# Optimization experiments

Hardware: AMD Instinct MI355X
Metric: run time of the kernel (lower is better)

The kernel has to match this reference:

```python
import jax, jax.numpy as jnp
import numpy as np

C_IN, C_OUT, K = 64, 64, 3
KK = K * K


def _conv3x3(x, w, b):
    # x: [B, Cin, H, W], w: [Cout, Cin, 3, 3], b: [Cout] or None. stride 1, pad 1.
    y = jax.lax.conv_general_dilated(
        x, w, window_strides=(1, 1), padding=((1, 1), (1, 1)),
        dimension_numbers=("NCHW", "OIHW", "NCHW"))
    if b is not None:
        y = y + b[None, :, None, None]
    return y


def _deform_conv2d(x, offset, mask, weight):
    # torchvision.ops.deform_conv2d with stride=1, pad=1, dilation=1, 1 offset group.
    # x: [B,C,H,W]; offset: [B,2*KK,H,W] (per-tap (dy,dx)); mask: [B,KK,H,W];
    # weight: [O,C,K,K]
    B, C, H, W = x.shape
    O = weight.shape[0]
    ky, kx = jnp.meshgrid(jnp.arange(K), jnp.arange(K), indexing="ij")
    hs = jnp.arange(H)
    ws = jnp.arange(W)
    # base sample positions per tap k=(ky*K+kx): [KK,H,W]
    base_y = (hs[:, None] - 1)[None] + ky.reshape(KK, 1, 1)
    base_x = (ws[None, :] - 1)[None] + kx.reshape(KK, 1, 1)
    off = offset.reshape(B, KK, 2, H, W)
    py = base_y[None].astype(x.dtype) + off[:, :, 0]  # [B,KK,H,W]
    px = base_x[None].astype(x.dtype) + off[:, :, 1]

    y0 = jnp.floor(py)
    x0 = jnp.floor(px)
    wy = py - y0  # bilinear fractional weights
    wx = px - x0
    y0i = y0.astype(jnp.int32)
    x0i = x0.astype(jnp.int32)

    imflat = x.reshape(B, C, H * W)

    def gather_b(im, idx):  # im: [C,HW], idx: [KK,H,W] -> [C,KK,H,W]
        return im[:, idx]

    val = jnp.zeros((B, C, KK, H, W), x.dtype)
    for dy, dx in ((0, 0), (0, 1), (1, 0), (1, 1)):
        yc = y0i + dy
        xc = x0i + dx
        valid = ((yc >= 0) & (yc < H) & (xc >= 0) & (xc < W)).astype(x.dtype)
        cw = (wy if dy else (1.0 - wy)) * (wx if dx else (1.0 - wx)) * valid
        idx = jnp.clip(yc, 0, H - 1) * W + jnp.clip(xc, 0, W - 1)
        g = jax.vmap(gather_b)(imflat, idx)  # [B,C,KK,H,W]
        val = val + cw[:, None] * g
    val = val * mask[:, None]  # modulation
    # contract 9-tap patches with conv weight
    return jnp.einsum("bckhw,ock->bohw", val, weight.reshape(O, C, KK))


def setup_inputs() -> dict:
    key = jax.random.key(0)
    ks = jax.random.split(key, 8)
    B, H, W = 4, 96, 96
    cin2 = 2 * C_IN + 2
    frame_i = jax.random.normal(ks[0], (B, C_IN, H, W), jnp.float32)
    frame_j = jax.random.normal(ks[1], (B, C_IN, H, W), jnp.float32)
    flow_ij = jax.random.normal(ks[2], (B, 2, H, W), jnp.float32)
    # small random weights so offsets are nonzero (zero-init would degenerate)
    w_off = jax.random.normal(ks[3], (2 * KK, cin2, K, K), jnp.float32) * 0.01
    b_off = jax.random.normal(ks[4], (2 * KK,), jnp.float32) * 0.1
    w_mod = jax.random.normal(ks[5], (KK, cin2, K, K), jnp.float32) * 0.01
    b_mod = jax.random.normal(ks[6], (KK,), jnp.float32) * 0.1
    w_reg = jax.random.normal(ks[7], (C_OUT, C_IN, K, K), jnp.float32) * (1.0 / np.sqrt(C_IN * KK))
    return {"frame_i": frame_i, "frame_j": frame_j, "flow_ij": flow_ij,
            "w_off": w_off, "b_off": b_off, "w_mod": w_mod, "b_mod": b_mod,
            "w_reg": w_reg}


def reference(frame_i, frame_j, flow_ij, w_off, b_off, w_mod, b_mod, w_reg):
    offset_input = jnp.concatenate([frame_i, frame_j, flow_ij], axis=1)
    offset = _conv3x3(offset_input, w_off, b_off)            # [B,2*KK,H,W]
    modulator = 2.0 * jax.nn.sigmoid(_conv3x3(offset_input, w_mod, b_mod))  # [B,KK,H,W]
    return _deform_conv2d(frame_j, offset, modulator, w_reg)
```

## Files before the change

kernel.cpp:

```cpp
#include <hip/hip_runtime.h>
#include <math.h>

#define BB   4
#define HH   96
#define WW   96
#define HW   (HH * WW)
#define CIN  64
#define COUT 64
#define C2B  192
#define NROW (BB * HW)
#define ZROW NROW
#define NSTRIP (NROW / 16)
#define BPX3 (NSTRIP / 8)
#define NA   (9 * 5 * 2 * 512)
#define NW   (9 * 2 * 4 * 512)
#define PXB2 (NROW / 32)
#define PWBLK 324
#define TSX  35
#define PR   55

typedef short v8s __attribute__((ext_vector_type(8)));
typedef float v4f __attribute__((ext_vector_type(4)));

__device__ __forceinline__ unsigned short f2bf(float f) {
    unsigned u = __float_as_uint(f);
    return (unsigned short)((u + 0x7FFFu + ((u >> 16) & 1u)) >> 16);
}
__device__ __forceinline__ unsigned pack2(float a, float b) {
    return (unsigned)f2bf(a) | ((unsigned)f2bf(b) << 16);
}
__device__ __forceinline__ unsigned bil2(unsigned a, unsigned b, unsigned c,
                                         unsigned d, float w00, float w01,
                                         float w10, float w11) {
    float lo = w00 * __uint_as_float(a << 16) + w01 * __uint_as_float(b << 16)
             + w10 * __uint_as_float(c << 16) + w11 * __uint_as_float(d << 16);
    float hi = w00 * __uint_as_float(a & 0xffff0000u)
             + w01 * __uint_as_float(b & 0xffff0000u)
             + w10 * __uint_as_float(c & 0xffff0000u)
             + w11 * __uint_as_float(d & 0xffff0000u);
    return pack2(lo, hi);
}

__global__ __launch_bounds__(256) void prep_kernel(
    const float* __restrict__ fi, const float* __restrict__ fj,
    const float* __restrict__ fl, const float* __restrict__ w_off,
    const float* __restrict__ w_mod, const float* __restrict__ w_reg,
    unsigned short* __restrict__ xt, unsigned short* __restrict__ wa2f,
    unsigned short* __restrict__ wb2f, uint4* __restrict__ vt)
{
    int blk = blockIdx.x;
    if (blk < PXB2) {
        __shared__ __align__(16) unsigned tile[64 * TSX];
        int tid = threadIdx.x;
        int p = tid & 63, cg = tid >> 6;
        int u = blk >> 1, half = blk & 1;
        int r0 = u * 64;
        int b = r0 / HW;
        int hwb = r0 - b * HW;
        int hw = hwb + p;
        uint4* dst = (uint4*)(xt + (size_t)r0 * C2B);
        if (half == 0) {
            const float* pi = fi + (size_t)b * CIN * HW + hw;
#pragma unroll
            for (int d = 0; d < 8; ++d) {
                int c = cg * 16 + 2 * d;
                tile[p * TSX + cg * 8 + d] =
                    pack2(pi[(size_t)c * HW], pi[(size_t)(c + 1) * HW]);
            }
            __syncthreads();
#pragma unroll
            for (int i = 0; i < 2; ++i) {
                int gq = i * 256 + tid;
                int rl = gq >> 3, c4 = gq & 7;
                const unsigned* s = &tile[rl * TSX + c4 * 4];
                uint4 v = {s[0], s[1], s[2], s[3]};
                dst[rl * 24 + c4] = v;
            }
        } else {
            const float* pj = fj + (size_t)b * CIN * HW + hw;
#pragma unroll
            for (int d = 0; d < 8; ++d) {
                int c = cg * 16 + 2 * d;
                tile[p * TSX + cg * 8 + d] =
                    pack2(pj[(size_t)c * HW], pj[(size_t)(c + 1) * HW]);
            }
            if (cg == 0) {
                const float* pf = fl + (size_t)b * 2 * HW + hw;
                tile[p * TSX + 32] = pack2(pf[0], pf[HW]);
            }
            __syncthreads();
#pragma unroll
            for (int i = 0; i < 4; ++i) {
                int gq = i * 256 + tid;
                int rl = gq >> 4, c4 = gq & 15;
                uint4 v = {0u, 0u, 0u, 0u};
                if (c4 < 8) {
                    const unsigned* s = &tile[rl * TSX + c4 * 4];
                    v.x = s[0]; v.y = s[1]; v.z = s[2]; v.w = s[3];
                } else if (c4 == 8) {
                    v.x = tile[rl * TSX + 32];
                }
                int pc4 = (c4 < 8) ? ((c4 & 3) * 2 + (c4 >> 2)) : c4;
                dst[rl * 24 + 8 + pc4] = v;
            }
#pragma unroll
            for (int i = 0; i < 2; ++i) {
                int it = i * 256 + tid;
                int pl = it >> 6, rl = it & 63;
                int o  = (pl >> 1) + (pl & 1) * 4;
                const unsigned* s = &tile[rl * TSX + o * 4];
                uint4 v = {s[0], s[1], s[2], s[3]};
                vt[((size_t)(b * 8 + pl)) * HW + hwb + rl] = v;
            }
        }
    } else if (blk < PXB2 + PWBLK) {
        int e = (blk - PXB2) * 256 + threadIdx.x;
        if (e < NA) {
            int t  = e / 5120;
            int r1 = e - t * 5120;
            int ks = r1 >> 10;
            int r2 = r1 & 1023;
            int nt = r2 >> 9;
            int l9 = r2 & 511;
            int l  = l9 >> 3, ee = l9 & 7;
            int m  = l & 15, g = l >> 4;
            int oc = nt * 16 + m;
            int ch = ks * 32 + g * 8 + ee;
            float v = 0.0f;
            if (oc < 27 && ch < 130) {
                if (oc < 18) v = w_off[((size_t)oc * 130 + ch) * 9 + t];
                else         v = w_mod[((size_t)(oc - 18) * 130 + ch) * 9 + t];
            }
            wa2f[e] = f2bf(v);
        } else {
            int e2 = e - NA;
            if (e2 < NW) {
                int k  = e2 >> 12;
                int r1 = e2 & 4095;
                int ks = r1 >> 11;
                int r2 = r1 & 2047;
                int nt = r2 >> 9;
                int l9 = r2 & 511;
                int l  = l9 >> 3, ee = l9 & 7;
                int m  = l & 15, g = l >> 4;
                int o  = nt * 16 + m;
                int c  = ks * 32 + g * 8 + ee;
                wb2f[e2] = f2bf(w_reg[((size_t)o * 64 + c) * 9 + k]);
            }
        }
    } else {
        if (threadIdx.x < 24) {
            uint4 z = {0u, 0u, 0u, 0u};
            ((uint4*)(xt + (size_t)ZROW * C2B))[threadIdx.x] = z;
        }
    }
}

__global__ __launch_bounds__(512, 4) void fused_kernel(
    const unsigned short* __restrict__ xt,
    const unsigned short* __restrict__ wa2f,
    const unsigned short* __restrict__ wb2f,
    const uint4* __restrict__ vt,
    const float* __restrict__ b_off, const float* __restrict__ b_mod,
    float* __restrict__ out)
{
    __shared__ __align__(16) unsigned char pool[32768];
    __shared__ __align__(16) float red1[8][8][64];
    __shared__ float lraw[16 * 28];

    uint4* patch4 = (uint4*)pool;
    float* red2   = (float*)pool;

    int l = threadIdx.x & 63;
    int wid = __builtin_amdgcn_readfirstlane(threadIdx.x >> 6);
    int m = l & 15, g = l >> 4;
    int strip = (blockIdx.x & 7) * BPX3 + (blockIdx.x >> 3);
    int b = strip / (HW / 16);
    int hw0 = (strip - b * (HW / 16)) * 16;
    int hw = hw0 + m;
    int x = hw % WW, y = hw / WW;
    int y0b = hw0 / WW, x0b = hw0 - y0b * WW;

#pragma unroll
    for (int i = 0; i < 3; ++i) {
        int item = i * 512 + threadIdx.x;
        if (item < 1080) {
            int run = item / 360;
            int rem = item - run * 360;
            int r18 = rem / 20;
            int c8  = rem - r18 * 20;
            int yy = y0b + run - 1;
            int xx = x0b - 1 + r18;
            bool ok = ((unsigned)yy < HH) && ((unsigned)xx < WW);
            uint4 v = {0u, 0u, 0u, 0u};
            if (ok)
                v = ((const uint4*)(xt + (size_t)(b * HW + yy * WW + xx) * C2B))[c8];
            patch4[c8 * PR + run * 18 + r18] = v;
        }
    }
    __syncthreads();

    v4f acc0 = {0.f, 0.f, 0.f, 0.f};
    v4f acc1 = {0.f, 0.f, 0.f, 0.f};
    {
        int nu = (wid < 5) ? 6 : 5;
#pragma unroll
        for (int i = 0; i < 6; ++i) {
            if (i < nu) {
                int u = wid + 8 * i;
                int t = u / 5, ks = u - 5 * t;
                int r = (t / 3) * 18 + (t % 3) + m;
                int c8 = (ks == 0) ? g : (ks == 1) ? 4 + g
                       : (ks == 2) ? 8 + 2 * g : (ks == 3) ? 9 + 2 * g
                       : 16 + g;
                v8s a = *(const v8s*)&patch4[c8 * PR + r];
                const unsigned short* wp =
                    wa2f + ((size_t)(u * 2)) * 512 + l * 8;
                v8s b0 = *(const v8s*)(wp);
                v8s b1 = *(const v8s*)(wp + 512);
                acc0 = __builtin_amdgcn_mfma_f32_16x16x32_bf16(a, b0, acc0, 0, 0, 0);
                acc1 = __builtin_amdgcn_mfma_f32_16x16x32_bf16(a, b1, acc1, 0, 0, 0);
            }
        }
    }

    {
#pragma unroll
        for (int j = 0; j < 4; ++j) red1[wid][j][l] = acc0[j];
#pragma unroll
        for (int j = 0; j < 4; ++j) red1[wid][4 + j][l] = acc1[j];
    }
    __syncthreads();

    {
        int j = wid;
        float v = 0.f;
#pragma unroll
        for (int sw = 0; sw < 8; ++sw) v += red1[sw][j][l];
        int r = j & 3;
        int oc = (j < 4) ? m : 16 + m;
        int pos = g * 4 + r;
        if (oc < 18) {
            lraw[pos * 28 + oc] = v + b_off[oc];
        } else if (oc < 27) {
            lraw[pos * 28 + oc] =
                2.0f / (1.0f + __expf(-(v + b_mod[oc - 18])));
        }
    }
    __syncthreads();

    v4f acc[4];
#pragma unroll
    for (int nt = 0; nt < 4; ++nt) acc[nt] = (v4f){0.f, 0.f, 0.f, 0.f};

    const uint4* p0 = vt + ((size_t)(b * 8 + 2 * g + 0)) * HW;
    const uint4* p1 = vt + ((size_t)(b * 8 + 2 * g + 1)) * HW;

    auto do_tap = [&](int k) {
        int ky = k / 3, kx = k - 3 * ky;
        float dy = lraw[m * 28 + 2 * k];
        float dx = lraw[m * 28 + 2 * k + 1];
        float mm = lraw[m * 28 + 18 + k];

        float py = (float)(y - 1 + ky) + dy;
        float px = (float)(x - 1 + kx) + dx;
        float fy = floorf(py), fx = floorf(px);
        int   y0 = (int)fy,    x0 = (int)fx;
        float wy = py - fy,    wx = px - fx;
        int   y1 = y0 + 1,     x1 = x0 + 1;

        bool y0v = (y0 >= 0) && (y0 < HH);
        bool y1v = (y1 >= 0) && (y1 < HH);
        bool x0v = (x0 >= 0) && (x0 < WW);
        bool x1v = (x1 >= 0) && (x1 < WW);

        float w00 = (1.f - wy) * (1.f - wx) * ((y0v && x0v) ? mm : 0.f);
        float w01 = (1.f - wy) * wx         * ((y0v && x1v) ? mm : 0.f);
        float w10 = wy * (1.f - wx)         * ((y1v && x0v) ? mm : 0.f);
        float w11 = wy * wx                 * ((y1v && x1v) ? mm : 0.f);

        int y0c = min(max(y0, 0), HH - 1), y1c = min(max(y1, 0), HH - 1);
        int x0c = min(max(x0, 0), WW - 1), x1c = min(max(x1, 0), WW - 1);
        int i00 = y0c * WW + x0c, i01 = y0c * WW + x1c;
        int i10 = y1c * WW + x0c, i11 = y1c * WW + x1c;

        uint4 a00 = p0[i00];
        uint4 a01 = p0[i01];
        uint4 a10 = p0[i10];
        uint4 a11 = p0[i11];
        uint4 c00 = p1[i00];
        uint4 c01 = p1[i01];
        uint4 c10 = p1[i10];
        uint4 c11 = p1[i11];

        uint4 ov0, ov1;
        ov0.x = bil2(a00.x, a01.x, a10.x, a11.x, w00, w01, w10, w11);
        ov0.y = bil2(a00.y, a01.y, a10.y, a11.y, w00, w01, w10, w11);
        ov0.z = bil2(a00.z, a01.z, a10.z, a11.z, w00, w01, w10, w11);
        ov0.w = bil2(a00.w, a01.w, a10.w, a11.w, w00, w01, w10, w11);
        ov1.x = bil2(c00.x, c01.x, c10.x, c11.x, w00, w01, w10, w11);
        ov1.y = bil2(c00.y, c01.y, c10.y, c11.y, w00, w01, w10, w11);
        ov1.z = bil2(c00.z, c01.z, c10.z, c11.z, w00, w01, w10, w11);
        ov1.w = bil2(c00.w, c01.w, c10.w, c11.w, w00, w01, w10, w11);
        v8s af0 = __builtin_bit_cast(v8s, ov0);
        v8s af1 = __builtin_bit_cast(v8s, ov1);

#pragma unroll
        for (int nt = 0; nt < 4; ++nt) {
            const unsigned short* wp0 =
                wb2f + ((size_t)((k * 2 + 0) * 4 + nt)) * 512 + l * 8;
            const unsigned short* wp1 =
                wb2f + ((size_t)((k * 2 + 1) * 4 + nt)) * 512 + l * 8;
            v8s bb0 = *(const v8s*)wp0;
            v8s bb1 = *(const v8s*)wp1;
            acc[nt] = __builtin_amdgcn_mfma_f32_16x16x32_bf16(af0, bb0, acc[nt], 0, 0, 0);
            acc[nt] = __builtin_amdgcn_mfma_f32_16x16x32_bf16(af1, bb1, acc[nt], 0, 0, 0);
        }
    };

    do_tap(wid);
    if (wid == 7) do_tap(8);

    {
#pragma unroll
        for (int nt = 0; nt < 4; ++nt)
#pragma unroll
            for (int r = 0; r < 4; ++r)
                red2[((size_t)wid * 16 + nt * 4 + r) * 64 + l] = acc[nt][r];
    }
    __syncthreads();
    {
        int nt = wid >> 1, r0 = (wid & 1) * 2;
        float v0 = 0.f, v1 = 0.f;
#pragma unroll
        for (int sw = 0; sw < 8; ++sw) {
            v0 += red2[((size_t)sw * 16 + nt * 4 + r0) * 64 + l];
            v1 += red2[((size_t)sw * 16 + nt * 4 + r0 + 1) * 64 + l];
        }
        float* op = out + ((size_t)(b * COUT + nt * 16 + m)) * HW
                  + hw0 + g * 4 + r0;
        float2 s2 = {v0, v1};
        *(float2*)op = s2;
    }
}

extern "C" void kernel_launch(void* const* d_in, const int* in_sizes, int n_in,
                              void* d_out, int out_size, void* d_ws, size_t ws_size,
                              hipStream_t stream)
{
    const float* frame_i = (const float*)d_in[0];
    const float* frame_j = (const float*)d_in[1];
    const float* flow_ij = (const float*)d_in[2];
    const float* w_off   = (const float*)d_in[3];
    const float* b_off   = (const float*)d_in[4];
    const float* w_mod   = (const float*)d_in[5];
    const float* b_mod   = (const float*)d_in[6];
    const float* w_reg   = (const float*)d_in[7];
    float* out = (float*)d_out;

    unsigned short* xt   = (unsigned short*)d_ws;
    unsigned short* wa2f = xt + (size_t)(NROW + 1) * C2B;
    unsigned short* wb2f = wa2f + NA;
    uint4* vt            = (uint4*)(wb2f + NW);

    prep_kernel<<<PXB2 + PWBLK + 1, 256, 0, stream>>>(
        frame_i, frame_j, flow_ij, w_off, w_mod, w_reg, xt, wa2f, wb2f, vt);

    fused_kernel<<<NSTRIP, 512, 0, stream>>>(
        xt, wa2f, wb2f, vt, b_off, b_mod, out);
}
```

Before: 115.5 us.

## Shrink shared pool, split tap 8 across two waves, two-stage reduction

```diff
diff --git a/kernel.cpp b/kernel.cpp
--- a/kernel.cpp
+++ b/kernel.cpp
@@ -156,7 +156,7 @@
     }
 }
 
-__global__ __launch_bounds__(512, 4) void fused_kernel(
+__global__ __launch_bounds__(512, 8) void fused_kernel(
     const unsigned short* __restrict__ xt,
     const unsigned short* __restrict__ wa2f,
     const unsigned short* __restrict__ wb2f,
@@ -164,7 +164,7 @@
     const float* __restrict__ b_off, const float* __restrict__ b_mod,
     float* __restrict__ out)
 {
-    __shared__ __align__(16) unsigned char pool[32768];
+    __shared__ __align__(16) unsigned char pool[17600];
     __shared__ __align__(16) float red1[8][8][64];
     __shared__ float lraw[16 * 28];
 
@@ -253,9 +253,6 @@
 #pragma unroll
     for (int nt = 0; nt < 4; ++nt) acc[nt] = (v4f){0.f, 0.f, 0.f, 0.f};
 
-    const uint4* p0 = vt + ((size_t)(b * 8 + 2 * g + 0)) * HW;
-    const uint4* p1 = vt + ((size_t)(b * 8 + 2 * g + 1)) * HW;
-
     auto do_tap = [&](int k) {
         int ky = k / 3, kx = k - 3 * ky;
         float dy = lraw[m * 28 + 2 * k];
@@ -283,6 +280,9 @@
         int x0c = min(max(x0, 0), WW - 1), x1c = min(max(x1, 0), WW - 1);
         int i00 = y0c * WW + x0c, i01 = y0c * WW + x1c;
         int i10 = y1c * WW + x0c, i11 = y1c * WW + x1c;
+
+        const uint4* p0 = vt + ((size_t)(b * 8 + 2 * g + 0)) * HW;
+        const uint4* p1 = vt + ((size_t)(b * 8 + 2 * g + 1)) * HW;
 
         uint4 a00 = p0[i00];
         uint4 a01 = p0[i01];
@@ -318,24 +318,87 @@
         }
     };
 
+    auto do_half = [&](int k, int ks) {
+        int ky = k / 3, kx = k - 3 * ky;
+        float dy = lraw[m * 28 + 2 * k];
+        float dx = lraw[m * 28 + 2 * k + 1];
+        float mm = lraw[m * 28 + 18 + k];
+
+        float py = (float)(y - 1 + ky) + dy;
+        float px = (float)(x - 1 + kx) + dx;
+        float fy = floorf(py), fx = floorf(px);
+        int   y0 = (int)fy,    x0 = (int)fx;
+        float wy = py - fy,    wx = px - fx;
+        int   y1 = y0 + 1,     x1 = x0 + 1;
+
+        bool y0v = (y0 >= 0) && (y0 < HH);
+        bool y1v = (y1 >= 0) && (y1 < HH);
+        bool x0v = (x0 >= 0) && (x0 < WW);
+        bool x1v = (x1 >= 0) && (x1 < WW);
+
+        float w00 = (1.f - wy) * (1.f - wx) * ((y0v && x0v) ? mm : 0.f);
+        float w01 = (1.f - wy) * wx         * ((y0v && x1v) ? mm : 0.f);
+        float w10 = wy * (1.f - wx)         * ((y1v && x0v) ? mm : 0.f);
+        float w11 = wy * wx                 * ((y1v && x1v) ? mm : 0.f);
+
+        int y0c = min(max(y0, 0), HH - 1), y1c = min(max(y1, 0), HH - 1);
+        int x0c = min(max(x0, 0), WW - 1), x1c = min(max(x1, 0), WW - 1);
+        int i00 = y0c * WW + x0c, i01 = y0c * WW + x1c;
+        int i10 = y1c * WW + x0c, i11 = y1c * WW + x1c;
+
+        const uint4* pk = vt + ((size_t)(b * 8 + 2 * g + ks)) * HW;
+        uint4 a00 = pk[i00];
+        uint4 a01 = pk[i01];
+        uint4 a10 = pk[i10];
+        uint4 a11 = pk[i11];
+
+        uint4 ov;
+        ov.x = bil2(a00.x, a01.x, a10.x, a11.x, w00, w01, w10, w11);
+        ov.y = bil2(a00.y, a01.y, a10.y, a11.y, w00, w01, w10, w11);
+        ov.z = bil2(a00.z, a01.z, a10.z, a11.z, w00, w01, w10, w11);
+        ov.w = bil2(a00.w, a01.w, a10.w, a11.w, w00, w01, w10, w11);
+        v8s af = __builtin_bit_cast(v8s, ov);
+
+#pragma unroll
+        for (int nt = 0; nt < 4; ++nt) {
+            const unsigned short* wp =
+                wb2f + ((size_t)((k * 2 + ks) * 4 + nt)) * 512 + l * 8;
+            v8s bb = *(const v8s*)wp;
+            acc[nt] = __builtin_amdgcn_mfma_f32_16x16x32_bf16(af, bb, acc[nt], 0, 0, 0);
+        }
+    };
+
     do_tap(wid);
-    if (wid == 7) do_tap(8);
-
-    {
+    if (wid == 6) do_half(8, 0);
+    if (wid == 7) do_half(8, 1);
+
+    if (wid >= 4) {
+        float* rb = red2 + ((size_t)(wid - 4) * 16) * 64;
 #pragma unroll
         for (int nt = 0; nt < 4; ++nt)
 #pragma unroll
             for (int r = 0; r < 4; ++r)
-                red2[((size_t)wid * 16 + nt * 4 + r) * 64 + l] = acc[nt][r];
+                rb[(nt * 4 + r) * 64 + l] = acc[nt][r];
+    }
+    __syncthreads();
+    if (wid < 4) {
+        float* rb = red2 + ((size_t)wid * 16) * 64;
+#pragma unroll
+        for (int nt = 0; nt < 4; ++nt)
+#pragma unroll
+            for (int r = 0; r < 4; ++r) {
+                float t = rb[(nt * 4 + r) * 64 + l] + acc[nt][r];
+                rb[(nt * 4 + r) * 64 + l] = t;
+            }
     }
     __syncthreads();
     {
         int nt = wid >> 1, r0 = (wid & 1) * 2;
         float v0 = 0.f, v1 = 0.f;
 #pragma unroll
-        for (int sw = 0; sw < 8; ++sw) {
-            v0 += red2[((size_t)sw * 16 + nt * 4 + r0) * 64 + l];
-            v1 += red2[((size_t)sw * 16 + nt * 4 + r0 + 1) * 64 + l];
+        for (int bu = 0; bu < 4; ++bu) {
+            v0 += red2[((size_t)bu * 16 + nt * 4 + r0) * 64 + l];
+            v1 += red2[((size_t)bu * 16 + nt * 4 + r0 + 1) * 64 + l];
         }
         float* op = out + ((size_t)(b * COUT + nt * 16 + m)) * HW
                   + hw0 + g * 4 + r0;
```

After: 115.3 us. Within noise of the previous version (-0.2%).
